# Performance work log

Measured on AMD Instinct MI355X. Metric: run time of the kernel, lower is better.

The kernel has to match this reference:

```python
import jax, jax.numpy as jnp
import numpy as np


def setup_inputs() -> dict:
    key = jax.random.key(0)
    k1, k2, k3 = jax.random.split(key, 3)
    B, S, D = 4, 2048, 4096
    C, E = 8, 8  # num_clusters, experts per cluster
    hidden_states = jax.random.normal(k1, (B, S, D), dtype=jnp.float32)
    W_cluster = jax.random.normal(k2, (C, D), dtype=jnp.float32) * 0.02
    W_experts = jax.random.normal(k3, (C, E, D), dtype=jnp.float32) * 0.02
    expert_ids = jnp.arange(C * E, dtype=jnp.int64).reshape(C, E)
    return {"hidden_states": hidden_states, "W_cluster": W_cluster,
            "W_experts": W_experts, "expert_ids": expert_ids}


def reference(hidden_states, W_cluster, W_experts, expert_ids):
    # hidden_states: [B, S, D]; W_cluster: [C, D]; W_experts: [C, E, D]; expert_ids: [C, E]
    B, S, D = hidden_states.shape
    C, E, _ = W_experts.shape
    num_total = C * E
    x = hidden_states.reshape(-1, D)                      # [T, D]
    T = x.shape[0]
    # First-level: token-level top-1 cluster routing (cluster_token_routing=True).
    # softmax is monotone, so argmax over logits == argmax over softmax weights.
    cluster_logits = x @ W_cluster.T                      # [T, C]
    cluster_idx = jnp.argmax(cluster_logits, axis=-1)     # [T]
    # Second-level: expert logits for every cluster, then gather the chosen cluster's.
    all_logits = jnp.einsum('td,ced->tce', x, W_experts)  # [T, C, E]
    rows = jnp.arange(T)
    sel_logits = all_logits[rows, cluster_idx]            # [T, E]
    cols = expert_ids[cluster_idx]                        # [T, E] global expert slots
    neg_min = jnp.finfo(hidden_states.dtype).min
    routing = jnp.full((T, num_total), neg_min, dtype=hidden_states.dtype)
    routing = routing.at[rows[:, None], cols].set(sel_logits)
    return routing.reshape(B, S, num_total)
```

## Files before the change

### kernel.cpp

```cpp
#include <hip/hip_runtime.h>
#include <cfloat>

#define DDIM 4096
#define NCLUS 8
#define NEXP 8
#define NOUT 64
#define NW 72
#define NCOL 80
#define FILL_BITS 0xFF7F0000u

typedef float floatx4 __attribute__((ext_vector_type(4)));
typedef short bf16x8 __attribute__((ext_vector_type(8)));

__device__ __forceinline__ short bfh(float f) {
  return (short)(__float_as_uint(f) >> 16);
}
__device__ __forceinline__ bf16x8 pack8(const float4& a, const float4& b) {
  bf16x8 r;
  r[0] = bfh(a.x); r[1] = bfh(a.y); r[2] = bfh(a.z); r[3] = bfh(a.w);
  r[4] = bfh(b.x); r[5] = bfh(b.y); r[6] = bfh(b.z); r[7] = bfh(b.w);
  return r;
}

__global__ __launch_bounds__(512, 4) void k_mfma(const float* __restrict__ x,
                                                 const float* __restrict__ Wc,
                                                 const float* __restrict__ We,
                                                 const int* __restrict__ eids32,
                                                 float* __restrict__ out) {
  __shared__ float s_acc[8][16 * NCOL];

  const int tid = threadIdx.x;
  const int lane = tid & 63;
  const int wave = tid >> 6;
  const int tile0 = blockIdx.x * 16;

  const int m = lane & 15;
  const int q = lane >> 4;
  const int kw = wave * 512 + q * 8;

  const float* xrow = x + (size_t)(tile0 + m) * DDIM + kw;

  floatx4 acc[5];
#pragma unroll
  for (int ct = 0; ct < 5; ++ct) acc[ct] = (floatx4){0.f, 0.f, 0.f, 0.f};

#pragma unroll 2
  for (int step = 0; step < 16; ++step) {
    const int kb = step * 32;
    const float4 a0 = *(const float4*)(xrow + kb);
    const float4 a1 = *(const float4*)(xrow + kb + 4);
    const bf16x8 af = pack8(a0, a1);

#pragma unroll
    for (int ct = 0; ct < 5; ++ct) {
      const int wrow = ct * 16 + m;
      float4 b0 = {0.f, 0.f, 0.f, 0.f}, b1 = {0.f, 0.f, 0.f, 0.f};
      if (wrow < NW) {
        const float* bp = (wrow < NCLUS)
                              ? (Wc + (size_t)wrow * DDIM)
                              : (We + (size_t)(wrow - NCLUS) * DDIM);
        b0 = *(const float4*)(bp + kw + kb);
        b1 = *(const float4*)(bp + kw + kb + 4);
      }
      const bf16x8 bf_ = pack8(b0, b1);
      acc[ct] = __builtin_amdgcn_mfma_f32_16x16x32_bf16(af, bf_, acc[ct], 0, 0, 0);
    }
  }

#pragma unroll
  for (int ct = 0; ct < 5; ++ct)
#pragma unroll
    for (int r = 0; r < 4; ++r)
      s_acc[wave][(q * 4 + r) * NCOL + ct * 16 + m] = acc[ct][r];
  __syncthreads();

  for (int i = tid; i < 16 * NCOL; i += 512) {
    float s = s_acc[0][i];
#pragma unroll
    for (int w = 1; w < 8; ++w) s += s_acc[w][i];
    s_acc[0][i] = s;
  }
  __syncthreads();

  const int is64 = (eids32[1] == 0) ? 1 : 0;
  const float fillv = __uint_as_float(FILL_BITS);
  for (int idx = tid; idx < 16 * NOUT; idx += 512) {
    const int tok = idx >> 6;
    const int col = idx & 63;
    const float* P = &s_acc[0][tok * NCOL];
    float best = P[0];
    int c = 0;
#pragma unroll
    for (int cc = 1; cc < NCLUS; ++cc)
      if (P[cc] > best) { best = P[cc]; c = cc; }
    float val = fillv;
#pragma unroll
    for (int e = 0; e < NEXP; ++e) {
      const int slot = c * NEXP + e;
      const int ce = is64 ? eids32[slot << 1] : eids32[slot];
      if (ce == col) val = P[NCLUS + slot];
    }
    out[(size_t)(tile0 + tok) * NOUT + col] = val;
  }
}

extern "C" void kernel_launch(void* const* d_in, const int* in_sizes, int n_in,
                              void* d_out, int out_size, void* d_ws, size_t ws_size,
                              hipStream_t stream) {
  const float* x = (const float*)d_in[0];
  const float* Wc = (const float*)d_in[1];
  const float* We = (const float*)d_in[2];
  const int* eids = (const int*)d_in[3];
  float* out = (float*)d_out;

  const int T = in_sizes[0] / DDIM;
  k_mfma<<<T / 16, 512, 0, stream>>>(x, Wc, We, eids, out);
}
```

Before: 240.6 us.

## Prepack weights to bf16 MFMA fragments in workspace and software-prefetch loads

Adds a small pre-kernel that converts the cluster and expert weights once per call into bf16 fragments laid out in MFMA lane order in the workspace. The main kernel then reads one 16-byte fragment per tile instead of two float4 loads plus conversion. The K loop is also restructured to prefetch the next step's x and weight data into registers before issuing the current MFMAs. This cuts weight bandwidth and conversion work in every block, at the cost of an extra kernel launch and higher register pressure from double-buffering.

```diff
diff --git a/kernel.cpp b/kernel.cpp
--- a/kernel.cpp
+++ b/kernel.cpp
@@ -8,6 +8,7 @@
 #define NW 72
 #define NCOL 80
 #define FILL_BITS 0xFF7F0000u
+#define WS_BYTES (8 * 16 * 5 * 64 * 16)
 
 typedef float floatx4 __attribute__((ext_vector_type(4)));
 typedef short bf16x8 __attribute__((ext_vector_type(8)));
@@ -22,10 +23,35 @@
   return r;
 }
 
+__global__ __launch_bounds__(256) void k_pack(const float* __restrict__ Wc,
+                                              const float* __restrict__ We,
+                                              bf16x8* __restrict__ ws) {
+  const int gtid = blockIdx.x * 256 + threadIdx.x;
+  const int frag = gtid >> 6;
+  const int lane = gtid & 63;
+  const int w = frag / 80;
+  const int rem = frag % 80;
+  const int s = rem / 5;
+  const int ct = rem % 5;
+  const int row = ct * 16 + (lane & 15);
+  const int k = w * 512 + s * 32 + (lane >> 4) * 8;
+
+  float4 b0 = {0.f, 0.f, 0.f, 0.f}, b1 = {0.f, 0.f, 0.f, 0.f};
+  if (row < NW) {
+    const float* rp = (row < NCLUS) ? (Wc + (size_t)row * DDIM)
+                                    : (We + (size_t)(row - NCLUS) * DDIM);
+    b0 = *(const float4*)(rp + k);
+    b1 = *(const float4*)(rp + k + 4);
+  }
+  ws[gtid] = pack8(b0, b1);
+}
+
+template <bool USE_WS>
 __global__ __launch_bounds__(512, 4) void k_mfma(const float* __restrict__ x,
                                                  const float* __restrict__ Wc,
                                                  const float* __restrict__ We,
                                                  const int* __restrict__ eids32,
+                                                 const bf16x8* __restrict__ bws,
                                                  float* __restrict__ out) {
   __shared__ float s_acc[8][16 * NCOL];
 
@@ -39,32 +65,65 @@
   const int kw = wave * 512 + q * 8;
 
   const float* xrow = x + (size_t)(tile0 + m) * DDIM + kw;
+  const bf16x8* bbase = USE_WS ? (bws + (size_t)wave * 16 * 5 * 64 + lane) : nullptr;
 
   floatx4 acc[5];
 #pragma unroll
   for (int ct = 0; ct < 5; ++ct) acc[ct] = (floatx4){0.f, 0.f, 0.f, 0.f};
 
-#pragma unroll 2
-  for (int step = 0; step < 16; ++step) {
-    const int kb = step * 32;
-    const float4 a0 = *(const float4*)(xrow + kb);
-    const float4 a1 = *(const float4*)(xrow + kb + 4);
-    const bf16x8 af = pack8(a0, a1);
+  float4 pa0 = *(const float4*)(xrow);
+  float4 pa1 = *(const float4*)(xrow + 4);
+  bf16x8 pb[5];
+  float4 pb0[5], pb1[5];
+#pragma unroll
+  for (int ct = 0; ct < 5; ++ct) {
+    if (USE_WS) {
+      pb[ct] = bbase[ct * 64];
+    } else {
+      const int wrow = ct * 16 + m;
+      pb0[ct] = (float4){0.f, 0.f, 0.f, 0.f};
+      pb1[ct] = (float4){0.f, 0.f, 0.f, 0.f};
+      if (wrow < NW) {
+        const float* bp = (wrow < NCLUS) ? (Wc + (size_t)wrow * DDIM)
+                                         : (We + (size_t)(wrow - NCLUS) * DDIM);
+        pb0[ct] = *(const float4*)(bp + kw);
+        pb1[ct] = *(const float4*)(bp + kw + 4);
+      }
+    }
+  }
 
 #pragma unroll
-    for (int ct = 0; ct < 5; ++ct) {
-      const int wrow = ct * 16 + m;
-      float4 b0 = {0.f, 0.f, 0.f, 0.f}, b1 = {0.f, 0.f, 0.f, 0.f};
-      if (wrow < NW) {
-        const float* bp = (wrow < NCLUS)
-                              ? (Wc + (size_t)wrow * DDIM)
-                              : (We + (size_t)(wrow - NCLUS) * DDIM);
-        b0 = *(const float4*)(bp + kw + kb);
-        b1 = *(const float4*)(bp + kw + kb + 4);
+  for (int step = 0; step < 16; ++step) {
+    const float4 ca0 = pa0, ca1 = pa1;
+    bf16x8 cb[5];
+#pragma unroll
+    for (int ct = 0; ct < 5; ++ct)
+      cb[ct] = USE_WS ? pb[ct] : pack8(pb0[ct], pb1[ct]);
+
+    if (step < 15) {
+      const int kb = (step + 1) * 32;
+      pa0 = *(const float4*)(xrow + kb);
+      pa1 = *(const float4*)(xrow + kb + 4);
+#pragma unroll
+      for (int ct = 0; ct < 5; ++ct) {
+        if (USE_WS) {
+          pb[ct] = bbase[((step + 1) * 5 + ct) * 64];
+        } else {
+          const int wrow = ct * 16 + m;
+          if (wrow < NW) {
+            const float* bp = (wrow < NCLUS) ? (Wc + (size_t)wrow * DDIM)
+                                             : (We + (size_t)(wrow - NCLUS) * DDIM);
+            pb0[ct] = *(const float4*)(bp + kw + kb);
+            pb1[ct] = *(const float4*)(bp + kw + kb + 4);
+          }
+        }
       }
-      const bf16x8 bf_ = pack8(b0, b1);
-      acc[ct] = __builtin_amdgcn_mfma_f32_16x16x32_bf16(af, bf_, acc[ct], 0, 0, 0);
     }
+
+    const bf16x8 af = pack8(ca0, ca1);
+#pragma unroll
+    for (int ct = 0; ct < 5; ++ct)
+      acc[ct] = __builtin_amdgcn_mfma_f32_16x16x32_bf16(af, cb[ct], acc[ct], 0, 0, 0);
   }
 
 #pragma unroll
@@ -114,5 +173,12 @@
   float* out = (float*)d_out;
 
   const int T = in_sizes[0] / DDIM;
-  k_mfma<<<T / 16, 512, 0, stream>>>(x, Wc, We, eids, out);
+
+  if (ws_size >= (size_t)WS_BYTES) {
+    bf16x8* bws = (bf16x8*)d_ws;
+    k_pack<<<160, 256, 0, stream>>>(Wc, We, bws);
+    k_mfma<true><<<T / 16, 512, 0, stream>>>(x, Wc, We, eids, bws, out);
+  } else {
+    k_mfma<false><<<T / 16, 512, 0, stream>>>(x, Wc, We, eids, nullptr, out);
+  }
 }
```

Result: faster. 206.1 us (-14.4%).
